# Optimization experiments

Hardware: AMD Instinct MI355X
Metric: run time of the kernel (lower is better)

The kernel has to match this reference:

```python
import jax, jax.numpy as jnp
import numpy as np

D, H, FF, E, K, B, S = 1024, 16, 4096, 8, 2, 2, 2048
EPS = 1e-5


def _layernorm(x, g, b):
    mu = x.mean(-1, keepdims=True)
    var = x.var(-1, keepdims=True)
    return (x - mu) * jax.lax.rsqrt(var + EPS) * g + b


def setup_inputs() -> dict:
    key = jax.random.key(0)
    ks = jax.random.split(key, 16)
    s = 0.02
    return {
        "x": jax.random.normal(ks[0], (B, S, D), dtype=jnp.float32),
        "in_proj_w": jax.random.normal(ks[1], (3 * D, D), dtype=jnp.float32) * s,
        "in_proj_b": jnp.zeros((3 * D,), jnp.float32),
        "out_proj_w": jax.random.normal(ks[2], (D, D), dtype=jnp.float32) * s,
        "out_proj_b": jnp.zeros((D,), jnp.float32),
        "ln1_g": jnp.ones((D,), jnp.float32),
        "ln1_b": jnp.zeros((D,), jnp.float32),
        "ln2_g": jnp.ones((D,), jnp.float32),
        "ln2_b": jnp.zeros((D,), jnp.float32),
        "gate_w": jax.random.normal(ks[3], (E, D), dtype=jnp.float32) * s,
        "gate_b": jnp.zeros((E,), jnp.float32),
        "w1": jax.random.normal(ks[4], (E, FF, D), dtype=jnp.float32) * s,
        "b1": jnp.zeros((E, FF), jnp.float32),
        "w2": jax.random.normal(ks[5], (E, D, FF), dtype=jnp.float32) * s,
        "b2": jnp.zeros((E, D), jnp.float32),
    }


def reference(x, in_proj_w, in_proj_b, out_proj_w, out_proj_b,
              ln1_g, ln1_b, ln2_g, ln2_b,
              gate_w, gate_b, w1, b1, w2, b2):
    b, s, d = x.shape
    hd = d // H
    # --- self-attention (pre-LN), dropout = identity (eval) ---
    normed = _layernorm(x, ln1_g, ln1_b)
    qkv = normed @ in_proj_w.T + in_proj_b            # [b,s,3d]
    q, k, v = jnp.split(qkv, 3, axis=-1)
    q = q.reshape(b, s, H, hd).transpose(0, 2, 1, 3)  # [b,h,s,hd]
    k = k.reshape(b, s, H, hd).transpose(0, 2, 1, 3)
    v = v.reshape(b, s, H, hd).transpose(0, 2, 1, 3)
    scores = jnp.einsum('bhqe,bhke->bhqk', q, k) / np.sqrt(hd)
    attn = jax.nn.softmax(scores, axis=-1)
    o = jnp.einsum('bhqk,bhke->bhqe', attn, v)
    o = o.transpose(0, 2, 1, 3).reshape(b, s, d)
    attn_out = o @ out_proj_w.T + out_proj_b
    x = x + attn_out
    present_kv = (normed, normed)
    # --- MoE FFN ---
    n2 = _layernorm(x, ln2_g, ln2_b)
    xf = n2.reshape(-1, d)                             # [T,d]
    T = xf.shape[0]
    logits = xf @ gate_w.T + gate_b                    # [T,E]
    probs = jax.nn.softmax(logits, axis=-1)
    top_v, top_i = jax.lax.top_k(probs, K)             # [T,K]
    top_v = top_v / top_v.sum(-1, keepdims=True)
    # combine weights per (token, expert); topk indices are unique per token
    cw = jnp.zeros((T, E), probs.dtype).at[jnp.arange(T)[:, None], top_i].add(top_v)
    # dense all-experts FFN (mathematically identical to masked gather/scatter)
    h = jnp.einsum('td,efd->etf', xf, w1) + b1[:, None, :]   # [E,T,FF]
    h = jax.nn.gelu(h, approximate=False)
    eo = jnp.einsum('etf,edf->etd', h, w2) + b2[:, None, :]  # [E,T,d]
    moe_out = jnp.einsum('te,etd->td', cw, eo)               # [T,d]
    out = x + moe_out.reshape(b, s, d)
    # --- load balance loss (Switch) ---
    top1 = jnp.argmax(probs, axis=-1)
    f = jnp.mean(jax.nn.one_hot(top1, E, dtype=probs.dtype), axis=0)
    P = probs.mean(axis=0)
    load_loss = 0.01 * E * jnp.sum(f * P)
    return out, load_loss, probs.reshape(b, s, E), present_kv[0]
```

## Files before the change

kernel.cpp:

```cpp
#include <hip/hip_runtime.h>
#include <math.h>

#define D_ 1024
#define H_ 16
#define HD_ 64
#define FF_ 4096
#define E_ 8
#define B_ 2
#define S_ 2048
#define T_ 4096
#define MAXROWS 9216
#define MAXTILES 72

typedef unsigned short u16;
typedef __attribute__((ext_vector_type(4))) float f32x4;
typedef __attribute__((ext_vector_type(8))) __bf16 bf16x8;
typedef __attribute__((ext_vector_type(8))) _Float16 f16x8;
typedef __attribute__((ext_vector_type(4))) unsigned short u16x4;

__device__ __forceinline__ u16 f2bf(float f){
  union { float f; unsigned u; } v; v.f = f;
  unsigned r = v.u + 0x7fffu + ((v.u >> 16) & 1u);
  return (u16)(r >> 16);
}
__device__ __forceinline__ float bf2f(u16 h){
  union { unsigned u; float f; } v; v.u = ((unsigned)h) << 16;
  return v.f;
}
__device__ __forceinline__ void glds16(const void* g, void* l){
  __builtin_amdgcn_global_load_lds((const __attribute__((address_space(1))) void*)g,
                                   (__attribute__((address_space(3))) void*)l, 16, 0, 0);
}
__device__ __forceinline__ bf16x8 ld8(const u16* p){
  return *reinterpret_cast<const bf16x8*>(p);
}
__device__ __forceinline__ f16x8 ldH8(const _Float16* p){
  return *reinterpret_cast<const f16x8*>(p);
}
__device__ __forceinline__ f32x4 mfma16(bf16x8 a, bf16x8 b, f32x4 c){
  return __builtin_amdgcn_mfma_f32_16x16x32_bf16(a, b, c, 0, 0, 0);
}
__device__ __forceinline__ f32x4 mfmaH(f16x8 a, f16x8 b, f32x4 c){
  return __builtin_amdgcn_mfma_f32_16x16x32_f16(a, b, c, 0, 0, 0);
}
__device__ __forceinline__ unsigned pk16(float a, float b){
  auto pk = __builtin_amdgcn_cvt_pkrtz(a, b);
  return __builtin_bit_cast(unsigned, pk);
}

__global__ void __launch_bounds__(256) split_hl_kernel(const float* __restrict__ in, u16* __restrict__ hi,
                                                       u16* __restrict__ lo, int n4){
  int i = blockIdx.x*blockDim.x + threadIdx.x;
  if (i >= n4) return;
  float4 v = reinterpret_cast<const float4*>(in)[i];
  float vv[4] = {v.x, v.y, v.z, v.w};
  u16x4 h, l;
  #pragma unroll
  for (int j=0;j<4;j++){
    u16 hh = f2bf(vv[j]);
    h[j] = hh;
    l[j] = f2bf(vv[j] - bf2f(hh));
  }
  reinterpret_cast<u16x4*>(hi)[i] = h;
  reinterpret_cast<u16x4*>(lo)[i] = l;
}

__global__ void __launch_bounds__(256) cvt_bf_kernel(const float* __restrict__ in, u16* __restrict__ out, int n4){
  int i = blockIdx.x*blockDim.x + threadIdx.x;
  if (i >= n4) return;
  float4 v = reinterpret_cast<const float4*>(in)[i];
  u16x4 o;
  o[0]=f2bf(v.x); o[1]=f2bf(v.y); o[2]=f2bf(v.z); o[3]=f2bf(v.w);
  reinterpret_cast<u16x4*>(out)[i] = o;
}

__global__ void __launch_bounds__(256) cvt_f16_kernel(const float* __restrict__ in, _Float16* __restrict__ out, int n4){
  int i = blockIdx.x*blockDim.x + threadIdx.x;
  if (i >= n4) return;
  float4 v = reinterpret_cast<const float4*>(in)[i];
  union { unsigned w[2]; u16x4 u; } o;
  o.w[0] = pk16(v.x, v.y);
  o.w[1] = pk16(v.z, v.w);
  reinterpret_cast<u16x4*>(out)[i] = o.u;
}

template<int OUTMODE>
__global__ void __launch_bounds__(256) ln_kernel(const float* __restrict__ x, const float* __restrict__ g,
    const float* __restrict__ bta, float* __restrict__ outf, u16* __restrict__ nout)
{
  const int t = blockIdx.x, tid = threadIdx.x;
  const float4 v = reinterpret_cast<const float4*>(x + (size_t)t*D_)[tid];
  float s  = v.x+v.y+v.z+v.w;
  float s2 = v.x*v.x+v.y*v.y+v.z*v.z+v.w*v.w;
  #pragma unroll
  for (int o=32;o;o>>=1){ s += __shfl_xor(s,o); s2 += __shfl_xor(s2,o); }
  __shared__ float rs[4], rq[4];
  const int wid=tid>>6, lane=tid&63;
  if (lane==0){ rs[wid]=s; rq[wid]=s2; }
  __syncthreads();
  s  = rs[0]+rs[1]+rs[2]+rs[3];
  s2 = rq[0]+rq[1]+rq[2]+rq[3];
  const float mu  = s*(1.0f/D_);
  const float var = s2*(1.0f/D_) - mu*mu;
  const float inv = rsqrtf(var + 1e-5f);
  const float4 gv = reinterpret_cast<const float4*>(g)[tid];
  const float4 bv = reinterpret_cast<const float4*>(bta)[tid];
  float oo[4];
  oo[0] = (v.x-mu)*inv*gv.x + bv.x;
  oo[1] = (v.y-mu)*inv*gv.y + bv.y;
  oo[2] = (v.z-mu)*inv*gv.z + bv.z;
  oo[3] = (v.w-mu)*inv*gv.w + bv.w;
  const size_t base = (size_t)t*D_ + tid*4;
  if (outf){ outf[base]=oo[0]; outf[base+1]=oo[1]; outf[base+2]=oo[2]; outf[base+3]=oo[3]; }
  if (OUTMODE==1){
    union { unsigned w[2]; u16x4 u; } hv;
    hv.w[0] = pk16(oo[0], oo[1]);
    hv.w[1] = pk16(oo[2], oo[3]);
    reinterpret_cast<u16x4*>(nout)[base>>2] = hv.u;
  } else {
    u16x4 hv;
    hv[0]=f2bf(oo[0]); hv[1]=f2bf(oo[1]); hv[2]=f2bf(oo[2]); hv[3]=f2bf(oo[3]);
    reinterpret_cast<u16x4*>(nout)[base>>2] = hv;
  }
}

__global__ void __launch_bounds__(256) qkv_kernel(
    const _Float16* __restrict__ A, const _Float16* __restrict__ Bw,
    const float* __restrict__ bias,
    _Float16* __restrict__ qf, _Float16* __restrict__ kf, _Float16* __restrict__ vtf)
{
  __shared__ __align__(16) _Float16 Ash[128*32], Bsh[128*32];
  const int tid=threadIdx.x, wid=tid>>6, lane=tid&63;
  const int wr=wid>>1, wc=wid&1;
  const int r16=lane&15, g4=lane>>4;
  const int nt=blockIdx.x, mt=blockIdx.y;
  const _Float16* Ag = A  + (size_t)mt*128*D_;
  const _Float16* Bg = Bw + (size_t)nt*128*D_;
  const int srow = wid*16 + (lane>>2);
  const int scol = (((lane&3) ^ ((lane>>3)&3)))*8;
  const int sl   = (g4 ^ ((r16>>1)&3))*8;
  f32x4 acc[4][4] = {};
  for (int k0=0;k0<D_;k0+=32){
    #pragma unroll
    for (int p=0;p<2;p++){
      const int r  = p*64 + srow;
      const int lo = (p*64 + wid*16)*32;
      glds16(Ag + (size_t)r*D_ + k0 + scol, &Ash[lo]);
      glds16(Bg + (size_t)r*D_ + k0 + scol, &Bsh[lo]);
    }
    __syncthreads();
    f16x8 af[4], bfr[4];
    #pragma unroll
    for (int m=0;m<4;m++) af[m]=ldH8(&Ash[(wr*64+m*16+r16)*32 + sl]);
    #pragma unroll
    for (int n=0;n<4;n++) bfr[n]=ldH8(&Bsh[(wc*64+n*16+r16)*32 + sl]);
    #pragma unroll
    for (int m=0;m<4;m++){
      #pragma unroll
      for (int n=0;n<4;n++) acc[m][n] = mfmaH(af[m], bfr[n], acc[m][n]);
    }
    __syncthreads();
  }
  #pragma unroll
  for (int m=0;m<4;m++){
    #pragma unroll
    for (int n=0;n<4;n++){
      #pragma unroll
      for (int r=0;r<4;r++){
        const int grow = mt*128 + wr*64 + m*16 + g4*4 + r;
        const int gcol = nt*128 + wc*64 + n*16 + r16;
        const float val = acc[m][n][r] + bias[gcol];
        const int which = gcol>>10, rem = gcol&1023;
        const int hh = rem>>6, ee = rem&63;
        const int bb = grow>>11, ss = grow&2047;
        if (which==0){
          qf[((size_t)(bb*H_+hh)*S_ + ss)*HD_ + ee] = (_Float16)(val * 0.18033688f);
        } else if (which==1){
          kf[((size_t)(bb*H_+hh)*S_ + ss)*HD_ + ee] = (_Float16)val;
        } else {
          const int p32 = 2*(ss & 12) + (ss & 3) + 4*((ss >> 4) & 1);
          const size_t idx = (((size_t)(bb*H_+hh)*(S_/32) + (ss>>5))*HD_ + ee)*32 + p32;
          vtf[idx] = (_Float16)val;
        }
      }
    }
  }
}

__global__ void __launch_bounds__(256) gemm3_kernel(
    const u16* __restrict__ Ah, const u16* __restrict__ Al, int lda,
    const u16* __restrict__ Bh, const u16* __restrict__ Bl, int Kdim,
    const float* __restrict__ bias,
    const float* __restrict__ resid, float* __restrict__ x1out)
{
  __shared__ __align__(16) u16 Ash[128*32], Asl[128*32], Bsh[128*32], Bsl[128*32];
  const int tid=threadIdx.x, wid=tid>>6, lane=tid&63;
  const int wr=wid>>1, wc=wid&1;
  const int r16=lane&15, g4=lane>>4;
  const int nt=blockIdx.x, mt=blockIdx.y;
  const u16* Agh = Ah + (size_t)mt*128*lda;
  const u16* Agl = Al + (size_t)mt*128*lda;
  const u16* Bgh = Bh + (size_t)nt*128*Kdim;
  const u16* Bgl = Bl + (size_t)nt*128*Kdim;
  const int srow = wid*16 + (lane>>2);
  const int scol = (((lane&3) ^ ((lane>>3)&3)))*8;
  const int sl   = (g4 ^ ((r16>>1)&3))*8;
  f32x4 acc[4][4] = {};
  for (int k0=0;k0<Kdim;k0+=32){
    #pragma unroll
    for (int p=0;p<2;p++){
      const int r  = p*64 + srow;
      const int lo = (p*64 + wid*16)*32;
      glds16(Agh + (size_t)r*lda  + k0 + scol, &Ash[lo]);
      glds16(Agl + (size_t)r*lda  + k0 + scol, &Asl[lo]);
      glds16(Bgh + (size_t)r*Kdim + k0 + scol, &Bsh[lo]);
      glds16(Bgl + (size_t)r*Kdim + k0 + scol, &Bsl[lo]);
    }
    __syncthreads();
    bf16x8 afh[4], afl[4], bfh[4], bfl[4];
    #pragma unroll
    for (int m=0;m<4;m++){
      const int row = wr*64 + m*16 + r16;
      afh[m] = ld8(&Ash[row*32 + sl]);
      afl[m] = ld8(&Asl[row*32 + sl]);
    }
    #pragma unroll
    for (int n=0;n<4;n++){
      const int row = wc*64 + n*16 + r16;
      bfh[n] = ld8(&Bsh[row*32 + sl]);
      bfl[n] = ld8(&Bsl[row*32 + sl]);
    }
    #pragma unroll
    for (int m=0;m<4;m++){
      #pragma unroll
      for (int n=0;n<4;n++){
        acc[m][n] = mfma16(afl[m], bfh[n], acc[m][n]);
        acc[m][n] = mfma16(afh[m], bfl[n], acc[m][n]);
        acc[m][n] = mfma16(afh[m], bfh[n], acc[m][n]);
      }
    }
    __syncthreads();
  }
  #pragma unroll
  for (int m=0;m<4;m++){
    #pragma unroll
    for (int n=0;n<4;n++){
      #pragma unroll
      for (int r=0;r<4;r++){
        const int grow = mt*128 + wr*64 + m*16 + g4*4 + r;
        const int gcol = nt*128 + wc*64 + n*16 + r16;
        const float val = acc[m][n][r] + bias[gcol];
        const size_t idx = (size_t)grow*D_ + gcol;
        x1out[idx] = val + resid[idx];
      }
    }
  }
}

__global__ void __launch_bounds__(256) attn7_kernel(
    const _Float16* __restrict__ Qf, const _Float16* __restrict__ Kf,
    const _Float16* __restrict__ Vtf,
    u16* __restrict__ Oh, u16* __restrict__ Ol)
{
  __shared__ __align__(16) _Float16 Kb[2][2048];
  __shared__ __align__(16) _Float16 Vb[2][2048];
  const int bid = blockIdx.x;
  const int wg = (bid & 7) * 128 + (bid >> 3);
  const int bh = wg >> 5, qc = wg & 31;
  const int tid=threadIdx.x, wid=tid>>6, lane=tid&63;
  const int r16=lane&15, g4=lane>>4;
  const int q0 = qc*64 + wid*16;
  const _Float16* Qp = Qf  + (size_t)bh*S_*HD_ + (size_t)(q0+r16)*HD_ + g4*8;
  const _Float16* Kbase = Kf  + (size_t)bh*S_*HD_;
  const _Float16* Vbase = Vtf + (size_t)bh*HD_*S_;
  const f16x8 qf0 = ldH8(Qp);
  const f16x8 qf1 = ldH8(Qp+32);
  f32x4 of[4] = {};
  float m_run = -3e38f, lr = 0.f;

  const int kOff = (wid*8 + (lane>>3))*HD_ + (((lane&7) ^ ((lane>>3)&7)))*8;
  const int vOff = wid*512 + lane*8;
  const int sk0 = (g4 ^ (r16&7))*8;
  const int sk1 = ((g4+4) ^ (r16&7))*8;

#define STAGE(bi, t) do { \
    glds16(Kbase + (size_t)(t)*32*HD_ + kOff, (void*)&Kb[bi][wid*512]); \
    glds16(Vbase + (size_t)(t)*2048   + vOff, (void*)&Vb[bi][wid*512]); \
  } while(0)

  STAGE(0, 0);
  asm volatile("s_waitcnt vmcnt(0)" ::: "memory");
  __syncthreads();
  int cur = 0;

  for (int t=0; t<64; ++t){
    if (t < 63) STAGE(cur^1, t+1);
    const _Float16* Kb_ = Kb[cur];
    const _Float16* Vb_ = Vb[cur];
    const f16x8 k0v = ldH8(Kb_ + r16*64 + sk0);
    const f16x8 k1v = ldH8(Kb_ + r16*64 + sk1);
    const f16x8 k2v = ldH8(Kb_ + (16+r16)*64 + sk0);
    const f16x8 k3v = ldH8(Kb_ + (16+r16)*64 + sk1);
    f32x4 sA={}, sB={};
    __builtin_amdgcn_s_setprio(1);
    sA = mfmaH(k0v, qf0, sA); sA = mfmaH(k1v, qf1, sA);
    sB = mfmaH(k2v, qf0, sB); sB = mfmaH(k3v, qf1, sB);
    __builtin_amdgcn_s_setprio(0);
    const float t0=sA[0], t1=sA[1], t2=sA[2], t3=sA[3];
    const float t4=sB[0], t5=sB[1], t6=sB[2], t7=sB[3];
    const float lmx = fmaxf(fmaxf(fmaxf(t0,t1),fmaxf(t2,t3)),
                            fmaxf(fmaxf(t4,t5),fmaxf(t6,t7)));
    if (!__all(lmx <= m_run + 4.0f)) {
      float mx = fmaxf(lmx, __shfl_xor(lmx,16));
      mx = fmaxf(mx, __shfl_xor(mx,32));
      const float mn = fmaxf(m_run, mx);
      const float alp = __builtin_amdgcn_exp2f(m_run - mn);
      m_run = mn;
      lr *= alp;
      const float ao0=__shfl(alp,4*g4), ao1=__shfl(alp,4*g4+1);
      const float ao2=__shfl(alp,4*g4+2), ao3=__shfl(alp,4*g4+3);
      #pragma unroll
      for (int c=0;c<4;c++){ of[c][0]*=ao0; of[c][1]*=ao1; of[c][2]*=ao2; of[c][3]*=ao3; }
    }
    const float msh = m_run - 9.0f;
    const float p0=__builtin_amdgcn_exp2f(t0-msh), p1=__builtin_amdgcn_exp2f(t1-msh);
    const float p2=__builtin_amdgcn_exp2f(t2-msh), p3=__builtin_amdgcn_exp2f(t3-msh);
    const float p4=__builtin_amdgcn_exp2f(t4-msh), p5=__builtin_amdgcn_exp2f(t5-msh);
    const float p6=__builtin_amdgcn_exp2f(t6-msh), p7=__builtin_amdgcn_exp2f(t7-msh);
    lr += ((p0+p1)+(p2+p3)) + ((p4+p5)+(p6+p7));
    union { unsigned w[4]; f16x8 v; } pu;
    pu.w[0]=pk16(p0,p1); pu.w[1]=pk16(p2,p3);
    pu.w[2]=pk16(p4,p5); pu.w[3]=pk16(p6,p7);
    const f16x8 v0v = ldH8(Vb_ + (r16)*32 + g4*8);
    const f16x8 v1v = ldH8(Vb_ + (16+r16)*32 + g4*8);
    const f16x8 v2v = ldH8(Vb_ + (32+r16)*32 + g4*8);
    const f16x8 v3v = ldH8(Vb_ + (48+r16)*32 + g4*8);
    __builtin_amdgcn_s_setprio(1);
    of[0] = mfmaH(pu.v, v0v, of[0]); of[1] = mfmaH(pu.v, v1v, of[1]);
    of[2] = mfmaH(pu.v, v2v, of[2]); of[3] = mfmaH(pu.v, v3v, of[3]);
    __builtin_amdgcn_s_setprio(0);
    asm volatile("s_waitcnt vmcnt(0)" ::: "memory");
    __syncthreads();
    cur ^= 1;
  }
#undef STAGE

  lr += __shfl_xor(lr,16);
  lr += __shfl_xor(lr,32);
  float li[4];
  #pragma unroll
  for (int r=0;r<4;r++) li[r] = 1.0f / __shfl(lr, 4*g4+r);
  const int bb = bh>>4, hh = bh&15;
  #pragma unroll
  for (int c=0;c<4;c++){
    #pragma unroll
    for (int r=0;r<4;r++){
      const float val = of[c][r] * li[r];
      const int qq = q0 + 4*g4 + r;
      const size_t idx = ((size_t)(bb*S_+qq))*D_ + hh*HD_ + c*16 + r16;
      const u16 hi = f2bf(val);
      Oh[idx]=hi; Ol[idx]=f2bf(val-bf2f(hi));
    }
  }
}

__global__ void __launch_bounds__(64) gate_kernel(
    const float* __restrict__ x1, const float* __restrict__ g2, const float* __restrict__ b2v,
    const float* __restrict__ gw, const float* __restrict__ gb,
    float* __restrict__ probs_out, int* __restrict__ top_i, float* __restrict__ cw_w)
{
  const int t = blockIdx.x, lane = threadIdx.x;
  const float* row = x1 + (size_t)t*D_;
  float xv[16];
  float s=0.f, s2=0.f;
  #pragma unroll
  for (int j=0;j<4;j++){
    float4 v = reinterpret_cast<const float4*>(row)[lane*4+j];
    xv[j*4]=v.x; xv[j*4+1]=v.y; xv[j*4+2]=v.z; xv[j*4+3]=v.w;
    s += v.x+v.y+v.z+v.w; s2 += v.x*v.x+v.y*v.y+v.z*v.z+v.w*v.w;
  }
  #pragma unroll
  for (int o=32;o;o>>=1){ s+=__shfl_xor(s,o); s2+=__shfl_xor(s2,o); }
  const float mu=s*(1.f/D_), var=s2*(1.f/D_)-mu*mu, inv=rsqrtf(var+1e-5f);
  float nv[16];
  #pragma unroll
  for (int j=0;j<4;j++){
    float4 gv = reinterpret_cast<const float4*>(g2)[lane*4+j];
    float4 bv = reinterpret_cast<const float4*>(b2v)[lane*4+j];
    nv[j*4]  =(xv[j*4]  -mu)*inv*gv.x+bv.x;
    nv[j*4+1]=(xv[j*4+1]-mu)*inv*gv.y+bv.y;
    nv[j*4+2]=(xv[j*4+2]-mu)*inv*gv.z+bv.z;
    nv[j*4+3]=(xv[j*4+3]-mu)*inv*gv.w+bv.w;
  }
  float acc[E_] = {};
  #pragma unroll
  for (int e=0;e<E_;e++){
    const float* w = gw + (size_t)e*D_ + lane*16;
    #pragma unroll
    for (int j=0;j<4;j++){
      float4 wv = reinterpret_cast<const float4*>(w)[j];
      acc[e] += nv[j*4]*wv.x + nv[j*4+1]*wv.y + nv[j*4+2]*wv.z + nv[j*4+3]*wv.w;
    }
  }
  #pragma unroll
  for (int e=0;e<E_;e++){
    #pragma unroll
    for (int o=32;o;o>>=1) acc[e]+=__shfl_xor(acc[e],o);
  }
  float lg[E_], mx=-3e38f;
  #pragma unroll
  for (int e=0;e<E_;e++){ lg[e]=acc[e]+gb[e]; mx=fmaxf(mx,lg[e]); }
  float ex[E_], sm=0.f;
  #pragma unroll
  for (int e=0;e<E_;e++){ ex[e]=__expf(lg[e]-mx); sm+=ex[e]; }
  float p[E_];
  #pragma unroll
  for (int e=0;e<E_;e++) p[e]=ex[e]/sm;
  if (lane<E_) probs_out[(size_t)t*E_+lane]=p[lane];
  int i0=0; float l0=lg[0];
  #pragma unroll
  for (int e=1;e<E_;e++) if (lg[e]>l0){ l0=lg[e]; i0=e; }
  int i1=-1; float l1=-3e38f;
  #pragma unroll
  for (int e=0;e<E_;e++) if (e!=i0 && lg[e]>l1){ l1=lg[e]; i1=e; }
  if (lane==0){
    top_i[2*t]=i0; top_i[2*t+1]=i1;
    const float v0=p[i0], v1=p[i1];
    const float swt=v0+v1;
    cw_w[2*t]=v0/swt; cw_w[2*t+1]=v1/swt;
  }
}

__global__ void __launch_bounds__(512) scan_kernel(const int* __restrict__ top_i,
    int* __restrict__ goff, int* __restrict__ tile_expert,
    int* __restrict__ assign_token, int* __restrict__ pos_of)
{
  __shared__ int cnt[E_];
  __shared__ int off[E_+1];
  const int tid=threadIdx.x;
  if (tid<E_) cnt[tid]=0;
  __syncthreads();
  for (int t=tid;t<T_;t+=512){
    atomicAdd(&cnt[top_i[2*t]],1);
    atomicAdd(&cnt[top_i[2*t+1]],1);
  }
  __syncthreads();
  if (tid==0){
    off[0]=0;
    for (int e=0;e<E_;e++) off[e+1]=off[e]+((cnt[e]+127)&~127);
    for (int i=0;i<=E_;i++) goff[i]=off[i];
  }
  __syncthreads();
  if (tid<MAXTILES){
    const int r=tid*128; int e=-1;
    for (int j=0;j<E_;j++) if (r>=off[j] && r<off[j+1]) e=j;
    tile_expert[tid]=e;
  }
  const int lane=tid&63;
  const int e=tid>>6;
  int base=off[e];
  for (int c=0;c<T_/64;c++){
    const int t=c*64+lane;
    const int a0=top_i[2*t], a1=top_i[2*t+1];
    const bool f=(a0==e)||(a1==e);
    const unsigned long long m=__ballot(f);
    if (f){
      const int pos = base + (int)__popcll(m & ((1ull<<lane)-1ull));
      assign_token[pos]=t;
      pos_of[2*t + (a0==e?0:1)] = pos;
    }
    base += (int)__popcll(m);
  }
  for (int r=base+lane; r<off[e+1]; r+=64) assign_token[r]=-1;
  __syncthreads();
  for (int r=off[E_]+tid; r<MAXROWS; r+=512) assign_token[r]=-1;
}

__global__ void __launch_bounds__(256) gather_kernel(const int* __restrict__ assign_token,
    const u16* __restrict__ n2b, u16* __restrict__ xg)
{
  const int r = blockIdx.x;
  const int t = assign_token[r];
  u16x4 val = {};
  if (t>=0) val = reinterpret_cast<const u16x4*>(n2b + (size_t)t*D_)[threadIdx.x];
  reinterpret_cast<u16x4*>(xg + (size_t)r*D_)[threadIdx.x] = val;
}

template<int MODE>
__global__ void __launch_bounds__(256) gemm_grp_kernel(
    const u16* __restrict__ A, int lda,
    const u16* __restrict__ Bbase, int Kdim, int Nsz,
    const float* __restrict__ bias,
    const int* __restrict__ tile_expert,
    u16* __restrict__ outp)
{
  const int nt=blockIdx.x, mt=blockIdx.y;
  const int e = tile_expert[mt];
  if (e<0) return;
  __shared__ __align__(16) u16 Ash[128*32], Bsh[128*32];
  const int tid=threadIdx.x, wid=tid>>6, lane=tid&63;
  const int wr=wid>>1, wc=wid&1;
  const int r16=lane&15, g4=lane>>4;
  const u16* Ag = A + (size_t)mt*128*lda;
  const u16* Bg = Bbase + (size_t)e*Nsz*Kdim + (size_t)nt*128*Kdim;
  const float* bp = bias + (size_t)e*Nsz;
  const int srow = wid*16 + (lane>>2);
  const int scol = (((lane&3) ^ ((lane>>3)&3)))*8;
  const int sl   = (g4 ^ ((r16>>1)&3))*8;
  f32x4 acc[4][4] = {};
  for (int k0=0;k0<Kdim;k0+=32){
    #pragma unroll
    for (int p=0;p<2;p++){
      const int r  = p*64+srow;
      const int lo = (p*64+wid*16)*32;
      glds16(Ag + (size_t)r*lda  + k0 + scol, &Ash[lo]);
      glds16(Bg + (size_t)r*Kdim + k0 + scol, &Bsh[lo]);
    }
    __syncthreads();
    bf16x8 af[4], bfr[4];
    #pragma unroll
    for (int m=0;m<4;m++) af[m]=ld8(&Ash[(wr*64+m*16+r16)*32 + sl]);
    #pragma unroll
    for (int n=0;n<4;n++) bfr[n]=ld8(&Bsh[(wc*64+n*16+r16)*32 + sl]);
    #pragma unroll
    for (int m=0;m<4;m++){
      #pragma unroll
      for (int n=0;n<4;n++) acc[m][n] = mfma16(af[m], bfr[n], acc[m][n]);
    }
    __syncthreads();
  }
  #pragma unroll
  for (int m=0;m<4;m++){
    #pragma unroll
    for (int n=0;n<4;n++){
      #pragma unroll
      for (int r=0;r<4;r++){
        const int grow = mt*128 + wr*64 + m*16 + g4*4 + r;
        const int gcol = nt*128 + wc*64 + n*16 + r16;
        float val = acc[m][n][r] + bp[gcol];
        if (MODE==2){
          const float z = val*(1.0f + 0.044715f*val*val)*2.3021622f;
          val = val / (1.0f + __builtin_amdgcn_exp2f(-z));
        }
        outp[(size_t)grow*Nsz + gcol] = f2bf(val);
      }
    }
  }
}

__global__ void __launch_bounds__(256) combine_kernel(const float* __restrict__ x1,
    const u16* __restrict__ eo, const int* __restrict__ pos_of, const float* __restrict__ cw_w,
    float* __restrict__ out0)
{
  const int t=blockIdx.x, tid=threadIdx.x;
  const int r0=pos_of[2*t], r1=pos_of[2*t+1];
  const float w0=cw_w[2*t], w1=cw_w[2*t+1];
  const u16x4 e0 = reinterpret_cast<const u16x4*>(eo + (size_t)r0*D_)[tid];
  const u16x4 e1 = reinterpret_cast<const u16x4*>(eo + (size_t)r1*D_)[tid];
  const float4 xv = reinterpret_cast<const float4*>(x1 + (size_t)t*D_)[tid];
  float4 o;
  o.x = xv.x + w0*bf2f(e0[0]) + w1*bf2f(e1[0]);
  o.y = xv.y + w0*bf2f(e0[1]) + w1*bf2f(e1[1]);
  o.z = xv.z + w0*bf2f(e0[2]) + w1*bf2f(e1[2]);
  o.w = xv.w + w0*bf2f(e0[3]) + w1*bf2f(e1[3]);
  reinterpret_cast<float4*>(out0 + (size_t)t*D_)[tid] = o;
}

__global__ void __launch_bounds__(256) loss_kernel(const float* __restrict__ probs,
    const int* __restrict__ top_i, float* __restrict__ loss_out)
{
  const int tid=threadIdx.x;
  float f[E_]={0,0,0,0,0,0,0,0}, P[E_]={0,0,0,0,0,0,0,0};
  for (int t=tid;t<T_;t+=256){
    const float* pr = probs + (size_t)t*E_;
    const int a0 = top_i[2*t];
    #pragma unroll
    for (int e=0;e<E_;e++){
      P[e] += pr[e];
      f[e] += (a0==e) ? 1.0f : 0.0f;
    }
  }
  #pragma unroll
  for (int e=0;e<E_;e++){
    #pragma unroll
    for (int o=32;o;o>>=1){ f[e]+=__shfl_xor(f[e],o); P[e]+=__shfl_xor(P[e],o); }
  }
  __shared__ float sf[4][E_], sP[4][E_];
  const int wid=tid>>6, lane=tid&63;
  if (lane==0){
    #pragma unroll
    for (int e=0;e<E_;e++){ sf[wid][e]=f[e]; sP[wid][e]=P[e]; }
  }
  __syncthreads();
  if (tid==0){
    float loss=0.f;
    #pragma unroll
    for (int e=0;e<E_;e++){
      const float fe=sf[0][e]+sf[1][e]+sf[2][e]+sf[3][e];
      const float Pe=sP[0][e]+sP[1][e]+sP[2][e]+sP[3][e];
      loss += (fe/(float)T_)*(Pe/(float)T_);
    }
    loss_out[0] = 0.01f*(float)E_*loss;
  }
}

static inline size_t alup(size_t x){ return (x+255)&~(size_t)255; }

extern "C" void kernel_launch(void* const* d_in, const int* in_sizes, int n_in,
                              void* d_out, int out_size, void* d_ws, size_t ws_size,
                              hipStream_t stream) {
  (void)in_sizes; (void)n_in; (void)out_size; (void)ws_size;
  const float* x    = (const float*)d_in[0];
  const float* ipw  = (const float*)d_in[1];
  const float* ipb  = (const float*)d_in[2];
  const float* opw  = (const float*)d_in[3];
  const float* opb  = (const float*)d_in[4];
  const float* ln1g = (const float*)d_in[5];
  const float* ln1b = (const float*)d_in[6];
  const float* ln2g = (const float*)d_in[7];
  const float* ln2b = (const float*)d_in[8];
  const float* gw   = (const float*)d_in[9];
  const float* gb   = (const float*)d_in[10];
  const float* w1   = (const float*)d_in[11];
  const float* b1   = (const float*)d_in[12];
  const float* w2   = (const float*)d_in[13];
  const float* b2   = (const float*)d_in[14];

  float* out0       = (float*)d_out;
  float* loss_out   = out0 + (size_t)T_*D_;
  float* probs_out  = loss_out + 1;
  float* normed_out = probs_out + (size_t)T_*E_;

  char* p = (char*)d_ws;
  auto take = [&](size_t bytes)->void*{ void* r = (void*)p; p += alup(bytes); return r; };

  _Float16* wipf = (_Float16*)take((size_t)3*D_*D_*2);
  u16* wop_h = (u16*)take((size_t)D_*D_*2);
  u16* wop_l = (u16*)take((size_t)D_*D_*2);
  u16* w1b   = (u16*)take((size_t)E_*FF_*D_*2);
  u16* w2b   = (u16*)take((size_t)E_*D_*FF_*2);
  _Float16* nf16 = (_Float16*)take((size_t)T_*D_*2);
  _Float16* qf  = (_Float16*)take((size_t)T_*D_*2);
  _Float16* kf  = (_Float16*)take((size_t)T_*D_*2);
  _Float16* vtf = (_Float16*)take((size_t)T_*D_*2);
  u16* oh    = (u16*)take((size_t)T_*D_*2);
  u16* ol    = (u16*)take((size_t)T_*D_*2);
  float* x1  = (float*)take((size_t)T_*D_*4);
  u16* n2b   = (u16*)take((size_t)T_*D_*2);
  u16* xg    = (u16*)take((size_t)MAXROWS*D_*2);
  u16* hbuf  = (u16*)take((size_t)MAXROWS*FF_*2);
  u16* eo    = (u16*)take((size_t)MAXROWS*D_*2);
  int* top_i = (int*)take((size_t)T_*2*4);
  float* cww = (float*)take((size_t)T_*2*4);
  int* posof = (int*)take((size_t)T_*2*4);
  int* goff  = (int*)take((size_t)(E_+1)*4);
  int* texp  = (int*)take((size_t)MAXTILES*4);
  int* atok  = (int*)take((size_t)MAXROWS*4);

  cvt_f16_kernel<<<(3*D_*D_/4+255)/256, 256, 0, stream>>>(ipw, wipf, 3*D_*D_/4);
  split_hl_kernel<<<(D_*D_/4+255)/256, 256, 0, stream>>>(opw, wop_h, wop_l, D_*D_/4);
  cvt_bf_kernel<<<(E_*FF_*D_/4+255)/256, 256, 0, stream>>>(w1, w1b, E_*FF_*D_/4);
  cvt_bf_kernel<<<(E_*D_*FF_/4+255)/256, 256, 0, stream>>>(w2, w2b, E_*D_*FF_/4);

  ln_kernel<1><<<T_, 256, 0, stream>>>(x, ln1g, ln1b, normed_out, (u16*)nf16);

  qkv_kernel<<<dim3(3*D_/128, T_/128), 256, 0, stream>>>(nf16, wipf, ipb, qf, kf, vtf);

  attn7_kernel<<<B_*H_*(S_/64), 256, 0, stream>>>(qf, kf, vtf, oh, ol);

  gemm3_kernel<<<dim3(D_/128, T_/128), 256, 0, stream>>>(
      oh, ol, D_, wop_h, wop_l, D_, opb, x, x1);

  ln_kernel<2><<<T_, 256, 0, stream>>>(x1, ln2g, ln2b, nullptr, n2b);

  gate_kernel<<<T_, 64, 0, stream>>>(x1, ln2g, ln2b, gw, gb, probs_out, top_i, cww);

  scan_kernel<<<1, 512, 0, stream>>>(top_i, goff, texp, atok, posof);

  gather_kernel<<<MAXROWS, 256, 0, stream>>>(atok, n2b, xg);

  gemm_grp_kernel<2><<<dim3(FF_/128, MAXTILES), 256, 0, stream>>>(xg, D_, w1b, D_, FF_, b1, texp, hbuf);
  gemm_grp_kernel<3><<<dim3(D_/128, MAXTILES), 256, 0, stream>>>(hbuf, FF_, w2b, FF_, D_, b2, texp, eo);

  combine_kernel<<<T_, 256, 0, stream>>>(x1, eo, posof, cww, out0);
  loss_kernel<<<1, 256, 0, stream>>>(probs_out, top_i, loss_out);
}
```

Before: 616.5 us.

## Double-buffer LDS in all GEMM kernels and remap blocks for XCD locality

Converts the qkv, out-proj, and grouped MoE GEMM kernels to double-buffered shared memory, so the global-to-LDS loads for the next K slice are issued before the MFMAs on the current one. Launches become 1D grids with a block-id remap that groups consecutive tiles per XCD (bid&7 stride), aiming for better L2 reuse across the 8 chiplets. The cost is doubled LDS use per block, which may lower occupancy, especially for gemm3 with four buffers. The explicit vmcnt(0) wait at the end of each iteration limits how much overlap is achieved.

```diff
diff --git a/kernel.cpp b/kernel.cpp
--- a/kernel.cpp
+++ b/kernel.cpp
@@ -129,38 +129,49 @@
     const float* __restrict__ bias,
     _Float16* __restrict__ qf, _Float16* __restrict__ kf, _Float16* __restrict__ vtf)
 {
-  __shared__ __align__(16) _Float16 Ash[128*32], Bsh[128*32];
+  __shared__ __align__(16) _Float16 Ash[2][128*32], Bsh[2][128*32];
+  const int bid = blockIdx.x, nwg = gridDim.x;
+  const int fid = (bid & 7)*(nwg>>3) + (bid>>3);
+  const int nt = fid % 24, mt = fid / 24;
   const int tid=threadIdx.x, wid=tid>>6, lane=tid&63;
   const int wr=wid>>1, wc=wid&1;
   const int r16=lane&15, g4=lane>>4;
-  const int nt=blockIdx.x, mt=blockIdx.y;
   const _Float16* Ag = A  + (size_t)mt*128*D_;
   const _Float16* Bg = Bw + (size_t)nt*128*D_;
   const int srow = wid*16 + (lane>>2);
   const int scol = (((lane&3) ^ ((lane>>3)&3)))*8;
   const int sl   = (g4 ^ ((r16>>1)&3))*8;
   f32x4 acc[4][4] = {};
-  for (int k0=0;k0<D_;k0+=32){
-    #pragma unroll
-    for (int p=0;p<2;p++){
-      const int r  = p*64 + srow;
-      const int lo = (p*64 + wid*16)*32;
-      glds16(Ag + (size_t)r*D_ + k0 + scol, &Ash[lo]);
-      glds16(Bg + (size_t)r*D_ + k0 + scol, &Bsh[lo]);
-    }
-    __syncthreads();
+#define QSTAGE(bi, k0) do { \
+    _Pragma("unroll") \
+    for (int p=0;p<2;p++){ \
+      const int r  = p*64 + srow; \
+      const int lo = (p*64 + wid*16)*32; \
+      glds16(Ag + (size_t)r*D_ + (k0) + scol, &Ash[bi][lo]); \
+      glds16(Bg + (size_t)r*D_ + (k0) + scol, &Bsh[bi][lo]); \
+    } \
+  } while(0)
+  QSTAGE(0, 0);
+  asm volatile("s_waitcnt vmcnt(0)" ::: "memory");
+  __syncthreads();
+  int cur = 0;
+  for (int t=0; t<D_/32; ++t){
+    if (t+1 < D_/32) QSTAGE(cur^1, (t+1)*32);
     f16x8 af[4], bfr[4];
     #pragma unroll
-    for (int m=0;m<4;m++) af[m]=ldH8(&Ash[(wr*64+m*16+r16)*32 + sl]);
-    #pragma unroll
-    for (int n=0;n<4;n++) bfr[n]=ldH8(&Bsh[(wc*64+n*16+r16)*32 + sl]);
+    for (int m=0;m<4;m++) af[m]=ldH8(&Ash[cur][(wr*64+m*16+r16)*32 + sl]);
+    #pragma unroll
+    for (int n=0;n<4;n++) bfr[n]=ldH8(&Bsh[cur][(wc*64+n*16+r16)*32 + sl]);
     #pragma unroll
     for (int m=0;m<4;m++){
       #pragma unroll
       for (int n=0;n<4;n++) acc[m][n] = mfmaH(af[m], bfr[n], acc[m][n]);
     }
+    asm volatile("s_waitcnt vmcnt(0)" ::: "memory");
     __syncthreads();
-  }
+    cur ^= 1;
+  }
+#undef QSTAGE
   #pragma unroll
   for (int m=0;m<4;m++){
     #pragma unroll
@@ -193,11 +204,13 @@
     const float* __restrict__ bias,
     const float* __restrict__ resid, float* __restrict__ x1out)
 {
-  __shared__ __align__(16) u16 Ash[128*32], Asl[128*32], Bsh[128*32], Bsl[128*32];
+  __shared__ __align__(16) u16 Ash[2][128*32], Asl[2][128*32], Bsh[2][128*32], Bsl[2][128*32];
+  const int bid = blockIdx.x, nwg = gridDim.x;
+  const int fid = (bid & 7)*(nwg>>3) + (bid>>3);
+  const int nt = fid & 7, mt = fid >> 3;
   const int tid=threadIdx.x, wid=tid>>6, lane=tid&63;
   const int wr=wid>>1, wc=wid&1;
   const int r16=lane&15, g4=lane>>4;
-  const int nt=blockIdx.x, mt=blockIdx.y;
   const u16* Agh = Ah + (size_t)mt*128*lda;
   const u16* Agl = Al + (size_t)mt*128*lda;
   const u16* Bgh = Bh + (size_t)nt*128*Kdim;
@@ -206,29 +219,36 @@
   const int scol = (((lane&3) ^ ((lane>>3)&3)))*8;
   const int sl   = (g4 ^ ((r16>>1)&3))*8;
   f32x4 acc[4][4] = {};
-  for (int k0=0;k0<Kdim;k0+=32){
-    #pragma unroll
-    for (int p=0;p<2;p++){
-      const int r  = p*64 + srow;
-      const int lo = (p*64 + wid*16)*32;
-      glds16(Agh + (size_t)r*lda  + k0 + scol, &Ash[lo]);
-      glds16(Agl + (size_t)r*lda  + k0 + scol, &Asl[lo]);
-      glds16(Bgh + (size_t)r*Kdim + k0 + scol, &Bsh[lo]);
-      glds16(Bgl + (size_t)r*Kdim + k0 + scol, &Bsl[lo]);
-    }
-    __syncthreads();
+#define G3STAGE(bi, k0) do { \
+    _Pragma("unroll") \
+    for (int p=0;p<2;p++){ \
+      const int r  = p*64 + srow; \
+      const int lo = (p*64 + wid*16)*32; \
+      glds16(Agh + (size_t)r*lda  + (k0) + scol, &Ash[bi][lo]); \
+      glds16(Agl + (size_t)r*lda  + (k0) + scol, &Asl[bi][lo]); \
+      glds16(Bgh + (size_t)r*Kdim + (k0) + scol, &Bsh[bi][lo]); \
+      glds16(Bgl + (size_t)r*Kdim + (k0) + scol, &Bsl[bi][lo]); \
+    } \
+  } while(0)
+  G3STAGE(0, 0);
+  asm volatile("s_waitcnt vmcnt(0)" ::: "memory");
+  __syncthreads();
+  int cur = 0;
+  const int NK = Kdim/32;
+  for (int t=0; t<NK; ++t){
+    if (t+1 < NK) G3STAGE(cur^1, (t+1)*32);
     bf16x8 afh[4], afl[4], bfh[4], bfl[4];
     #pragma unroll
     for (int m=0;m<4;m++){
       const int row = wr*64 + m*16 + r16;
-      afh[m] = ld8(&Ash[row*32 + sl]);
-      afl[m] = ld8(&Asl[row*32 + sl]);
+      afh[m] = ld8(&Ash[cur][row*32 + sl]);
+      afl[m] = ld8(&Asl[cur][row*32 + sl]);
     }
     #pragma unroll
     for (int n=0;n<4;n++){
       const int row = wc*64 + n*16 + r16;
-      bfh[n] = ld8(&Bsh[row*32 + sl]);
-      bfl[n] = ld8(&Bsl[row*32 + sl]);
+      bfh[n] = ld8(&Bsh[cur][row*32 + sl]);
+      bfl[n] = ld8(&Bsl[cur][row*32 + sl]);
     }
     #pragma unroll
     for (int m=0;m<4;m++){
@@ -239,8 +259,11 @@
         acc[m][n] = mfma16(afh[m], bfh[n], acc[m][n]);
       }
     }
+    asm volatile("s_waitcnt vmcnt(0)" ::: "memory");
     __syncthreads();
-  }
+    cur ^= 1;
+  }
+#undef G3STAGE
   #pragma unroll
   for (int m=0;m<4;m++){
     #pragma unroll
@@ -489,15 +512,17 @@
 template<int MODE>
 __global__ void __launch_bounds__(256) gemm_grp_kernel(
     const u16* __restrict__ A, int lda,
-    const u16* __restrict__ Bbase, int Kdim, int Nsz,
+    const u16* __restrict__ Bbase, int Kdim, int Nsz, int NT,
     const float* __restrict__ bias,
     const int* __restrict__ tile_expert,
     u16* __restrict__ outp)
 {
-  const int nt=blockIdx.x, mt=blockIdx.y;
+  const int bid = blockIdx.x, nwg = gridDim.x;
+  const int fid = (bid & 7)*(nwg>>3) + (bid>>3);
+  const int nt = fid % NT, mt = fid / NT;
   const int e = tile_expert[mt];
   if (e<0) return;
-  __shared__ __align__(16) u16 Ash[128*32], Bsh[128*32];
+  __shared__ __align__(16) u16 Ash[2][128*32], Bsh[2][128*32];
   const int tid=threadIdx.x, wid=tid>>6, lane=tid&63;
   const int wr=wid>>1, wc=wid&1;
   const int r16=lane&15, g4=lane>>4;
@@ -508,27 +533,37 @@
   const int scol = (((lane&3) ^ ((lane>>3)&3)))*8;
   const int sl   = (g4 ^ ((r16>>1)&3))*8;
   f32x4 acc[4][4] = {};
-  for (int k0=0;k0<Kdim;k0+=32){
-    #pragma unroll
-    for (int p=0;p<2;p++){
-      const int r  = p*64+srow;
-      const int lo = (p*64+wid*16)*32;
-      glds16(Ag + (size_t)r*lda  + k0 + scol, &Ash[lo]);
-      glds16(Bg + (size_t)r*Kdim + k0 + scol, &Bsh[lo]);
-    }
-    __syncthreads();
+#define GSTAGE(bi, k0) do { \
+    _Pragma("unroll") \
+    for (int p=0;p<2;p++){ \
+      const int r  = p*64+srow; \
+      const int lo = (p*64+wid*16)*32; \
+      glds16(Ag + (size_t)r*lda  + (k0) + scol, &Ash[bi][lo]); \
+      glds16(Bg + (size_t)r*Kdim + (k0) + scol, &Bsh[bi][lo]); \
+    } \
+  } while(0)
+  GSTAGE(0, 0);
+  asm volatile("s_waitcnt vmcnt(0)" ::: "memory");
+  __syncthreads();
+  int cur = 0;
+  const int NK = Kdim/32;
+  for (int t=0; t<NK; ++t){
+    if (t+1 < NK) GSTAGE(cur^1, (t+1)*32);
     bf16x8 af[4], bfr[4];
     #pragma unroll
-    for (int m=0;m<4;m++) af[m]=ld8(&Ash[(wr*64+m*16+r16)*32 + sl]);
-    #pragma unroll
-    for (int n=0;n<4;n++) bfr[n]=ld8(&Bsh[(wc*64+n*16+r16)*32 + sl]);
+    for (int m=0;m<4;m++) af[m]=ld8(&Ash[cur][(wr*64+m*16+r16)*32 + sl]);
+    #pragma unroll
+    for (int n=0;n<4;n++) bfr[n]=ld8(&Bsh[cur][(wc*64+n*16+r16)*32 + sl]);
     #pragma unroll
     for (int m=0;m<4;m++){
       #pragma unroll
       for (int n=0;n<4;n++) acc[m][n] = mfma16(af[m], bfr[n], acc[m][n]);
     }
+    asm volatile("s_waitcnt vmcnt(0)" ::: "memory");
     __syncthreads();
-  }
+    cur ^= 1;
+  }
+#undef GSTAGE
   #pragma unroll
   for (int m=0;m<4;m++){
     #pragma unroll
@@ -664,11 +699,11 @@
 
   ln_kernel<1><<<T_, 256, 0, stream>>>(x, ln1g, ln1b, normed_out, (u16*)nf16);
 
-  qkv_kernel<<<dim3(3*D_/128, T_/128), 256, 0, stream>>>(nf16, wipf, ipb, qf, kf, vtf);
+  qkv_kernel<<<dim3(24*(T_/128)), 256, 0, stream>>>(nf16, wipf, ipb, qf, kf, vtf);
 
   attn7_kernel<<<B_*H_*(S_/64), 256, 0, stream>>>(qf, kf, vtf, oh, ol);
 
-  gemm3_kernel<<<dim3(D_/128, T_/128), 256, 0, stream>>>(
+  gemm3_kernel<<<dim3(8*(T_/128)), 256, 0, stream>>>(
       oh, ol, D_, wop_h, wop_l, D_, opb, x, x1);
 
   ln_kernel<2><<<T_, 256, 0, stream>>>(x1, ln2g, ln2b, nullptr, n2b);
@@ -679,8 +714,8 @@
 
   gather_kernel<<<MAXROWS, 256, 0, stream>>>(atok, n2b, xg);
 
-  gemm_grp_kernel<2><<<dim3(FF_/128, MAXTILES), 256, 0, stream>>>(xg, D_, w1b, D_, FF_, b1, texp, hbuf);
-  gemm_grp_kernel<3><<<dim3(D_/128, MAXTILES), 256, 0, stream>>>(hbuf, FF_, w2b, FF_, D_, b2, texp, eo);
+  gemm_grp_kernel<2><<<dim3((FF_/128)*MAXTILES), 256, 0, stream>>>(xg, D_, w1b, D_, FF_, FF_/128, b1, texp, hbuf);
+  gemm_grp_kernel<3><<<dim3((D_/128)*MAXTILES), 256, 0, stream>>>(hbuf, FF_, w2b, FF_, D_, D_/128, b2, texp, eo);
 
   combine_kernel<<<T_, 256, 0, stream>>>(x1, eo, posof, cww, out0);
   loss_kernel<<<1, 256, 0, stream>>>(probs_out, top_i, loss_out);
```

New measurement: 546.8 us. -11.3%, faster.
